# Performance work log

Hardware: AMD Instinct MI355X
Metric: run time of the kernel (lower is better)

Reference implementation:

```python
import jax, jax.numpy as jnp
import numpy as np

N_NODES = 50000
N_EDGES = 800000
IN_CH = 256
H1, D1 = 4, 64   # layer 1: 4 heads x 64 -> 256
H2, D2 = 1, 64   # output layer: 1 head x 64
NEG_SLOPE = 0.2  # DGL GATConv default


def _leaky_relu(x):
    return jnp.where(x >= 0, x, NEG_SLOPE * x)


def gat_conv(h, src, dst, W, attn_l, attn_r, bias, res_W, num_heads, out_feats, apply_elu):
    """DGL GATConv (eval mode, feat_drop=attn_drop=0).
    h: (N, F_in); src/dst: (E,) edge endpoints (edge u->v aggregates at v).
    W: (F_in, H*D); attn_l/attn_r: (H, D); bias: (H*D,); res_W: (F_in, H*D) or None.
    Returns (N, H, D).
    """
    N = h.shape[0]
    ft = (h @ W).reshape(N, num_heads, out_feats)            # (N,H,D)
    el = jnp.sum(ft * attn_l, axis=-1)                        # (N,H)
    er = jnp.sum(ft * attn_r, axis=-1)                        # (N,H)
    e = _leaky_relu(el[src] + er[dst])                        # (E,H)
    # segment softmax over incoming edges of each dst node
    emax = jax.ops.segment_max(e, dst, num_segments=N)        # (N,H)
    emax = jax.lax.stop_gradient(emax)
    ee = jnp.exp(e - emax[dst])                               # (E,H)
    denom = jax.ops.segment_sum(ee, dst, num_segments=N)      # (N,H)
    a = ee / denom[dst]                                       # (E,H)
    msg = ft[src] * a[:, :, None]                             # (E,H,D)
    rst = jax.ops.segment_sum(msg, dst, num_segments=N)       # (N,H,D)
    if res_W is not None:
        rst = rst + (h @ res_W).reshape(N, num_heads, out_feats)
    rst = rst + bias.reshape(num_heads, out_feats)
    if apply_elu:
        rst = jax.nn.elu(rst)
    return rst


def setup_inputs() -> dict:
    key = jax.random.key(0)
    ks = jax.random.split(key, 12)
    feat = jax.random.normal(ks[0], (N_NODES, IN_CH), dtype=jnp.float32)
    src = jax.random.randint(ks[1], (N_EDGES,), 0, N_NODES)
    dst = jax.random.randint(ks[2], (N_EDGES,), 0, N_NODES)
    s = 0.1
    W1 = jax.random.normal(ks[3], (IN_CH, H1 * D1), dtype=jnp.float32) * s
    al1 = jax.random.normal(ks[4], (H1, D1), dtype=jnp.float32) * s
    ar1 = jax.random.normal(ks[5], (H1, D1), dtype=jnp.float32) * s
    b1 = jnp.zeros((H1 * D1,), dtype=jnp.float32)
    W2 = jax.random.normal(ks[6], (H1 * D1, H2 * D2), dtype=jnp.float32) * s
    al2 = jax.random.normal(ks[7], (H2, D2), dtype=jnp.float32) * s
    ar2 = jax.random.normal(ks[8], (H2, D2), dtype=jnp.float32) * s
    b2 = jnp.zeros((H2 * D2,), dtype=jnp.float32)
    resW2 = jax.random.normal(ks[9], (H1 * D1, H2 * D2), dtype=jnp.float32) * s
    return {"feat": feat, "src": src, "dst": dst,
            "W1": W1, "al1": al1, "ar1": ar1, "b1": b1,
            "W2": W2, "al2": al2, "ar2": ar2, "b2": b2, "resW2": resW2}


def reference(feat, src, dst, W1, al1, ar1, b1, W2, al2, ar2, b2, resW2):
    # Layer 1: 4 heads, ELU, no residual (first DGL layer built without residual)
    h = gat_conv(feat, src, dst, W1, al1, ar1, b1, None, H1, D1, True)
    h = h.reshape(N_NODES, H1 * D1)  # flatten(1)
    # Layer 2: 1 head, residual (linear res_fc since 256 != 64), no activation
    h = gat_conv(h, src, dst, W2, al2, ar2, b2, resW2, H2, D2, False)
    return h.mean(axis=1)  # mean over output heads -> (N, out_channels)
```

## Files before the change

### kernel.cpp

```cpp
#include <hip/hip_runtime.h>
#include <math.h>

#define N_NODES 50000
#define N_EDGES 800000
#define ELL_W 64

typedef __attribute__((ext_vector_type(8))) short bf16x8;
typedef __attribute__((ext_vector_type(4))) float f32x4;

__device__ __forceinline__ float leaky(float x) { return x >= 0.f ? x : 0.2f * x; }
__device__ __forceinline__ unsigned short f2bf(float f) {
  unsigned u = __float_as_uint(f);
  return (unsigned short)((u + 0x7fffu + ((u >> 16) & 1u)) >> 16);
}
__device__ __forceinline__ float bflo(unsigned u) { return __uint_as_float(u << 16); }
__device__ __forceinline__ float bfhi(unsigned u) { return __uint_as_float(u & 0xffff0000u); }
__device__ __forceinline__ unsigned pack2(float a, float b) {
  return (unsigned)f2bf(a) | ((unsigned)f2bf(b) << 16);
}

__launch_bounds__(256)
__global__ void prep_k(const float* __restrict__ feat, const float* __restrict__ W1,
                       const float* __restrict__ W2, const float* __restrict__ resW2,
                       short* __restrict__ featb, short* __restrict__ Wt1,
                       short* __restrict__ Wt2) {
  const int gtid = blockIdx.x * 256 + threadIdx.x;
  const int gsz = gridDim.x * 256;
  for (int idx = gtid; idx < 256 * 256; idx += gsz) {
    int n = idx >> 8, k = idx & 255;
    Wt1[idx] = (short)f2bf(W1[(size_t)k * 256 + n]);
  }
  for (int idx = gtid; idx < 128 * 256; idx += gsz) {
    int n = idx >> 8, k = idx & 255;
    float v = (n < 64) ? W2[(size_t)k * 64 + n] : resW2[(size_t)k * 64 + (n - 64)];
    Wt2[idx] = (short)f2bf(v);
  }
  const float4* f4 = (const float4*)feat;
  uint2* fb2 = (uint2*)featb;
  for (int idx = gtid; idx < N_NODES * 64; idx += gsz) {
    float4 f = f4[idx];
    uint2 o;
    o.x = pack2(f.x, f.y);
    o.y = pack2(f.z, f.w);
    fb2[idx] = o;
  }
}

template <int MODE, bool SCAT>
__launch_bounds__(256)
__global__ void mfma_gemm_k(const short* __restrict__ A, const short* __restrict__ Bt,
                            const float* __restrict__ bias, const float* __restrict__ al,
                            const float* __restrict__ ar, float* __restrict__ elp,
                            float* __restrict__ erp, short* __restrict__ Cb,
                            float* __restrict__ Cf, const int* __restrict__ src,
                            const int* __restrict__ dst, int* __restrict__ cnt,
                            int* __restrict__ ell, int M, int K, int N) {
  constexpr int EPI_COLS = (MODE == 0) ? 136 : 72;
  union SharedU {
    struct { short As[4][128][8]; short Bs[4][128][8]; } ab;
    short epi[128 * EPI_COLS];
  };
  __shared__ SharedU sh;

  if (SCAT && blockIdx.y == 2) {
    const int gtid = blockIdx.x * 256 + threadIdx.x;
    const int gsz = gridDim.x * 256;
    for (int e = gtid; e < N_EDGES; e += gsz) {
      int d = dst[e];
      int slot = atomicAdd(cnt + d, 1);
      if (slot < ELL_W) ell[d * ELL_W + slot] = src[e];
    }
    return;
  }
  const int tid = threadIdx.x;
  const int bm0 = blockIdx.x * 128, bn0 = blockIdx.y * 128;
  const int wave = tid >> 6, lane = tid & 63;
  const int wm = (wave & 1) * 64, wn = (wave >> 1) * 64;
  const int q = lane >> 4, r16 = lane & 15;
  const int srow = tid >> 1, sk = (tid & 1) * 16, sq = (tid & 1) * 2;
  f32x4 acc[4][4] = {};

  for (int k0 = 0; k0 < K; k0 += 32) {
    {
      uint4 v0 = {0, 0, 0, 0}, v1 = {0, 0, 0, 0};
      if (bm0 + srow < M) {
        const uint4* p = (const uint4*)(A + (size_t)(bm0 + srow) * K + k0 + sk);
        v0 = p[0];
        v1 = p[1];
      }
      *(uint4*)&sh.ab.As[sq][srow][0] = v0;
      *(uint4*)&sh.ab.As[sq + 1][srow][0] = v1;
    }
    {
      const uint4* p = (const uint4*)(Bt + (size_t)(bn0 + srow) * K + k0 + sk);
      *(uint4*)&sh.ab.Bs[sq][srow][0] = p[0];
      *(uint4*)&sh.ab.Bs[sq + 1][srow][0] = p[1];
    }
    __syncthreads();
    bf16x8 af[4], bfr[4];
#pragma unroll
    for (int i = 0; i < 4; ++i) af[i] = *(const bf16x8*)&sh.ab.As[q][wm + i * 16 + r16][0];
#pragma unroll
    for (int j = 0; j < 4; ++j) bfr[j] = *(const bf16x8*)&sh.ab.Bs[q][wn + j * 16 + r16][0];
#pragma unroll
    for (int i = 0; i < 4; ++i)
#pragma unroll
      for (int j = 0; j < 4; ++j)
        acc[i][j] = __builtin_amdgcn_mfma_f32_16x16x32_bf16(af[i], bfr[j], acc[i][j], 0, 0, 0);
    __syncthreads();
  }

  if (MODE == 0 || wn == 0) {
    const int head = (bn0 + wn) >> 6;
    float alv[4], arv[4];
#pragma unroll
    for (int j = 0; j < 4; ++j) {
      alv[j] = al[((MODE == 0) ? head * 64 : 0) + j * 16 + r16];
      arv[j] = ar[((MODE == 0) ? head * 64 : 0) + j * 16 + r16];
    }
#pragma unroll
    for (int i = 0; i < 4; ++i) {
#pragma unroll
      for (int reg = 0; reg < 4; ++reg) {
        float dl = acc[i][0][reg] * alv[0] + acc[i][1][reg] * alv[1] +
                   acc[i][2][reg] * alv[2] + acc[i][3][reg] * alv[3];
        float dr = acc[i][0][reg] * arv[0] + acc[i][1][reg] * arv[1] +
                   acc[i][2][reg] * arv[2] + acc[i][3][reg] * arv[3];
#pragma unroll
        for (int mm = 1; mm < 16; mm <<= 1) {
          dl += __shfl_xor(dl, mm);
          dr += __shfl_xor(dr, mm);
        }
        int row_g = bm0 + wm + i * 16 + q * 4 + reg;
        if (r16 == 0 && row_g < M) {
          if (MODE == 0) {
            elp[(size_t)row_g * 4 + head] = dl;
            erp[(size_t)row_g * 4 + head] = dr;
          } else {
            elp[row_g] = dl;
            erp[row_g] = dr;
          }
        }
      }
    }
  }

  if (MODE == 0) {
#pragma unroll
    for (int i = 0; i < 4; ++i)
#pragma unroll
      for (int reg = 0; reg < 4; ++reg) {
        int row = wm + i * 16 + q * 4 + reg;
#pragma unroll
        for (int j = 0; j < 4; ++j)
          sh.epi[row * EPI_COLS + wn + j * 16 + r16] = (short)f2bf(acc[i][j][reg]);
      }
    __syncthreads();
#pragma unroll
    for (int k = 0; k < 8; ++k) {
      int c = k * 256 + tid;
      int row = c >> 4, cc = c & 15;
      int row_g = bm0 + row;
      if (row_g < M) {
        uint4 v = *(const uint4*)&sh.epi[row * EPI_COLS + cc * 8];
        *(uint4*)(Cb + (size_t)row_g * N + bn0 + cc * 8) = v;
      }
    }
  } else {
    if (wn == 0) {
#pragma unroll
      for (int i = 0; i < 4; ++i)
#pragma unroll
        for (int reg = 0; reg < 4; ++reg) {
          int row = wm + i * 16 + q * 4 + reg;
#pragma unroll
          for (int j = 0; j < 4; ++j)
            sh.epi[row * EPI_COLS + j * 16 + r16] = (short)f2bf(acc[i][j][reg]);
        }
    } else {
#pragma unroll
      for (int i = 0; i < 4; ++i)
#pragma unroll
        for (int reg = 0; reg < 4; ++reg) {
          int row_g = bm0 + wm + i * 16 + q * 4 + reg;
          if (row_g >= M) continue;
#pragma unroll
          for (int j = 0; j < 4; ++j) {
            int col = j * 16 + r16;
            Cf[(size_t)row_g * 64 + col] = acc[i][j][reg] + bias[col];
          }
        }
    }
    __syncthreads();
#pragma unroll
    for (int k = 0; k < 4; ++k) {
      int c = k * 256 + tid;
      int row = c >> 3, cc = c & 7;
      int row_g = bm0 + row;
      if (row_g < M) {
        uint4 v = *(const uint4*)&sh.epi[row * EPI_COLS + cc * 8];
        *(uint4*)(Cb + (size_t)row_g * 64 + cc * 8) = v;
      }
    }
  }
}

__launch_bounds__(256)
__global__ void agg1_k(const int* __restrict__ ell, const int* __restrict__ cnt,
                       const float* __restrict__ el, const float* __restrict__ er,
                       const short* __restrict__ ft, const float* __restrict__ bias,
                       short* __restrict__ h1) {
  int node = blockIdx.x * 4 + (threadIdx.x >> 6);
  int lane = threadIdx.x & 63;
  if (node >= N_NODES) return;
  int deg = min(cnt[node], ELL_W);
  const int* row = ell + node * ELL_W;
  int h = lane >> 4;
  float erh = er[(size_t)node * 4 + h];
  float denom = 0.f;
  float4 acc = make_float4(0.f, 0.f, 0.f, 0.f);
  int i = 0;
  for (; i + 8 <= deg; i += 8) {
    int s[8];
#pragma unroll
    for (int k = 0; k < 8; ++k) s[k] = row[i + k];
    float e[8];
    uint2 u[8];
#pragma unroll
    for (int k = 0; k < 8; ++k) e[k] = leaky(el[(size_t)s[k] * 4 + h] + erh);
#pragma unroll
    for (int k = 0; k < 8; ++k) u[k] = *(const uint2*)(ft + (size_t)s[k] * 256 + lane * 4);
    float w[8];
#pragma unroll
    for (int k = 0; k < 8; ++k) w[k] = __expf(e[k]);
#pragma unroll
    for (int k = 0; k < 8; ++k) {
      denom += w[k];
      acc.x += w[k] * bflo(u[k].x);
      acc.y += w[k] * bfhi(u[k].x);
      acc.z += w[k] * bflo(u[k].y);
      acc.w += w[k] * bfhi(u[k].y);
    }
  }
  for (; i + 4 <= deg; i += 4) {
    int s0 = row[i + 0], s1 = row[i + 1], s2 = row[i + 2], s3 = row[i + 3];
    float e0 = leaky(el[(size_t)s0 * 4 + h] + erh);
    float e1 = leaky(el[(size_t)s1 * 4 + h] + erh);
    float e2 = leaky(el[(size_t)s2 * 4 + h] + erh);
    float e3 = leaky(el[(size_t)s3 * 4 + h] + erh);
    uint2 u0 = *(const uint2*)(ft + (size_t)s0 * 256 + lane * 4);
    uint2 u1 = *(const uint2*)(ft + (size_t)s1 * 256 + lane * 4);
    uint2 u2 = *(const uint2*)(ft + (size_t)s2 * 256 + lane * 4);
    uint2 u3 = *(const uint2*)(ft + (size_t)s3 * 256 + lane * 4);
    float w0 = __expf(e0), w1 = __expf(e1), w2 = __expf(e2), w3 = __expf(e3);
    denom += (w0 + w1) + (w2 + w3);
    acc.x += (w0 * bflo(u0.x) + w1 * bflo(u1.x)) + (w2 * bflo(u2.x) + w3 * bflo(u3.x));
    acc.y += (w0 * bfhi(u0.x) + w1 * bfhi(u1.x)) + (w2 * bfhi(u2.x) + w3 * bfhi(u3.x));
    acc.z += (w0 * bflo(u0.y) + w1 * bflo(u1.y)) + (w2 * bflo(u2.y) + w3 * bflo(u3.y));
    acc.w += (w0 * bfhi(u0.y) + w1 * bfhi(u1.y)) + (w2 * bfhi(u2.y) + w3 * bfhi(u3.y));
  }
  for (; i < deg; ++i) {
    int s = row[i];
    float e = leaky(el[(size_t)s * 4 + h] + erh);
    uint2 u = *(const uint2*)(ft + (size_t)s * 256 + lane * 4);
    float w = __expf(e);
    denom += w;
    acc.x += w * bflo(u.x);
    acc.y += w * bfhi(u.x);
    acc.z += w * bflo(u.y);
    acc.w += w * bfhi(u.y);
  }
  float inv = (deg > 0) ? 1.f / denom : 0.f;
  float4 b = *(const float4*)(bias + lane * 4);
  float4 v;
  v.x = acc.x * inv + b.x;
  v.y = acc.y * inv + b.y;
  v.z = acc.z * inv + b.z;
  v.w = acc.w * inv + b.w;
  v.x = v.x > 0.f ? v.x : expm1f(v.x);
  v.y = v.y > 0.f ? v.y : expm1f(v.y);
  v.z = v.z > 0.f ? v.z : expm1f(v.z);
  v.w = v.w > 0.f ? v.w : expm1f(v.w);
  uint2 o;
  o.x = pack2(v.x, v.y);
  o.y = pack2(v.z, v.w);
  *(uint2*)(h1 + (size_t)node * 256 + lane * 4) = o;
}

__launch_bounds__(256)
__global__ void agg2_k(const int* __restrict__ ell, const int* __restrict__ cnt,
                       const float* __restrict__ el, const float* __restrict__ er,
                       const short* __restrict__ ft, float* __restrict__ out) {
  int node = blockIdx.x * 4 + (threadIdx.x >> 6);
  int lane = threadIdx.x & 63;
  if (node >= N_NODES) return;
  int deg = min(cnt[node], ELL_W);
  const int* row = ell + node * ELL_W;
  float erd = er[node];
  float denom = 0.f, acc = 0.f;
  int i = 0;
  for (; i + 8 <= deg; i += 8) {
    int s[8];
#pragma unroll
    for (int k = 0; k < 8; ++k) s[k] = row[i + k];
    float e[8], f[8];
#pragma unroll
    for (int k = 0; k < 8; ++k) e[k] = leaky(el[s[k]] + erd);
#pragma unroll
    for (int k = 0; k < 8; ++k)
      f[k] = bflo((unsigned)(unsigned short)ft[(size_t)s[k] * 64 + lane]);
#pragma unroll
    for (int k = 0; k < 8; ++k) {
      float w = __expf(e[k]);
      denom += w;
      acc += w * f[k];
    }
  }
  for (; i < deg; ++i) {
    int s = row[i];
    float e = leaky(el[s] + erd);
    float f = bflo((unsigned)(unsigned short)ft[(size_t)s * 64 + lane]);
    float w = __expf(e);
    denom += w;
    acc += w * f;
  }
  float r = (deg > 0) ? acc / denom : 0.f;
  out[(size_t)node * 64 + lane] += r;
}

extern "C" void kernel_launch(void* const* d_in, const int* in_sizes, int n_in,
                              void* d_out, int out_size, void* d_ws, size_t ws_size,
                              hipStream_t stream) {
  const float* feat  = (const float*)d_in[0];
  const int*   src   = (const int*)d_in[1];
  const int*   dst   = (const int*)d_in[2];
  const float* W1    = (const float*)d_in[3];
  const float* al1   = (const float*)d_in[4];
  const float* ar1   = (const float*)d_in[5];
  const float* b1    = (const float*)d_in[6];
  const float* W2    = (const float*)d_in[7];
  const float* al2   = (const float*)d_in[8];
  const float* ar2   = (const float*)d_in[9];
  const float* b2    = (const float*)d_in[10];
  const float* resW2 = (const float*)d_in[11];
  float* out = (float*)d_out;

  char* p = (char*)d_ws;
  short* featb = (short*)p; p += (size_t)N_NODES * 256 * 2;
  short* ft1b = (short*)p; p += (size_t)N_NODES * 256 * 2;
  short* h1b  = (short*)p; p += (size_t)N_NODES * 256 * 2;
  short* ft2b = (short*)p; p += (size_t)N_NODES * 64 * 2;
  short* Wt1  = (short*)p; p += 256 * 256 * 2;
  short* Wt2  = (short*)p; p += 128 * 256 * 2;
  float* el1  = (float*)p; p += (size_t)N_NODES * 4 * 4;
  float* er1  = (float*)p; p += (size_t)N_NODES * 4 * 4;
  float* el2  = (float*)p; p += (size_t)N_NODES * 4;
  float* er2  = (float*)p; p += (size_t)N_NODES * 4;
  int* cnt    = (int*)p;   p += (size_t)N_NODES * 4;
  int* ell    = (int*)p;   p += (size_t)N_NODES * ELL_W * 4;

  hipMemsetAsync(cnt, 0, (size_t)N_NODES * sizeof(int), stream);

  dim3 blk(256);

  prep_k<<<2048, blk, 0, stream>>>(feat, W1, W2, resW2, featb, Wt1, Wt2);

  mfma_gemm_k<0, true><<<dim3(391, 3), blk, 0, stream>>>(
      featb, Wt1, nullptr, al1, ar1, el1, er1, ft1b, nullptr,
      src, dst, cnt, ell, N_NODES, 256, 256);
  agg1_k<<<12500, blk, 0, stream>>>(ell, cnt, el1, er1, ft1b, b1, h1b);

  mfma_gemm_k<1, false><<<dim3(391, 1), blk, 0, stream>>>(
      h1b, Wt2, b2, al2, ar2, el2, er2, ft2b, out,
      nullptr, nullptr, nullptr, nullptr, N_NODES, 256, 128);
  agg2_k<<<12500, blk, 0, stream>>>(ell, cnt, el2, er2, ft2b, out);
}
```

Before: 288.9 us.

## Split edge scatter across prep and GEMM kernels, store ELL as u16

The edge-to-ELL scatter is split in half: the first half runs in extra blocks of the prep kernel and the second half in the GEMM kernel's spare grid row. The ELL adjacency is stored as 16-bit source indices, which halves its footprint and the index reads in both aggregation kernels. The scatter now handles four edges per thread with vector loads and nontemporal stores. This relies on node ids fitting in 16 bits, and ordering within each ELL row now depends on interleaving across two kernels, which still gives correct results.

```diff
diff --git a/kernel.cpp b/kernel.cpp
--- a/kernel.cpp
+++ b/kernel.cpp
@@ -4,6 +4,10 @@
 #define N_NODES 50000
 #define N_EDGES 800000
 #define ELL_W 64
+
+#define E_SPLIT 400000
+#define CONV_BLKS 1792
+#define SCAT_BLKS 512
 
 typedef __attribute__((ext_vector_type(8))) short bf16x8;
 typedef __attribute__((ext_vector_type(4))) float f32x4;
@@ -19,13 +23,37 @@
   return (unsigned)f2bf(a) | ((unsigned)f2bf(b) << 16);
 }
 
+__device__ __forceinline__ void scat4(const int* __restrict__ src, const int* __restrict__ dst,
+                                      int* __restrict__ cnt, unsigned short* __restrict__ ell,
+                                      int e) {
+  int4 d4 = *(const int4*)(dst + e);
+  int4 s4 = *(const int4*)(src + e);
+  int sl;
+  sl = atomicAdd(cnt + d4.x, 1);
+  if (sl < ELL_W) __builtin_nontemporal_store((unsigned short)s4.x, ell + d4.x * ELL_W + sl);
+  sl = atomicAdd(cnt + d4.y, 1);
+  if (sl < ELL_W) __builtin_nontemporal_store((unsigned short)s4.y, ell + d4.y * ELL_W + sl);
+  sl = atomicAdd(cnt + d4.z, 1);
+  if (sl < ELL_W) __builtin_nontemporal_store((unsigned short)s4.z, ell + d4.z * ELL_W + sl);
+  sl = atomicAdd(cnt + d4.w, 1);
+  if (sl < ELL_W) __builtin_nontemporal_store((unsigned short)s4.w, ell + d4.w * ELL_W + sl);
+}
+
 __launch_bounds__(256)
 __global__ void prep_k(const float* __restrict__ feat, const float* __restrict__ W1,
                        const float* __restrict__ W2, const float* __restrict__ resW2,
                        short* __restrict__ featb, short* __restrict__ Wt1,
-                       short* __restrict__ Wt2) {
+                       short* __restrict__ Wt2, const int* __restrict__ src,
+                       const int* __restrict__ dst, int* __restrict__ cnt,
+                       unsigned short* __restrict__ ell) {
+  if (blockIdx.x >= CONV_BLKS) {
+    const int gtid = (blockIdx.x - CONV_BLKS) * 256 + threadIdx.x;
+    const int gsz = SCAT_BLKS * 256;
+    for (int q = gtid; q < E_SPLIT / 4; q += gsz) scat4(src, dst, cnt, ell, q * 4);
+    return;
+  }
   const int gtid = blockIdx.x * 256 + threadIdx.x;
-  const int gsz = gridDim.x * 256;
+  const int gsz = CONV_BLKS * 256;
   for (int idx = gtid; idx < 256 * 256; idx += gsz) {
     int n = idx >> 8, k = idx & 255;
     Wt1[idx] = (short)f2bf(W1[(size_t)k * 256 + n]);
@@ -54,7 +82,7 @@
                             float* __restrict__ erp, short* __restrict__ Cb,
                             float* __restrict__ Cf, const int* __restrict__ src,
                             const int* __restrict__ dst, int* __restrict__ cnt,
-                            int* __restrict__ ell, int M, int K, int N) {
+                            unsigned short* __restrict__ ell, int M, int K, int N) {
   constexpr int EPI_COLS = (MODE == 0) ? 136 : 72;
   union SharedU {
     struct { short As[4][128][8]; short Bs[4][128][8]; } ab;
@@ -65,11 +93,8 @@
   if (SCAT && blockIdx.y == 2) {
     const int gtid = blockIdx.x * 256 + threadIdx.x;
     const int gsz = gridDim.x * 256;
-    for (int e = gtid; e < N_EDGES; e += gsz) {
-      int d = dst[e];
-      int slot = atomicAdd(cnt + d, 1);
-      if (slot < ELL_W) ell[d * ELL_W + slot] = src[e];
-    }
+    for (int q = gtid; q < (N_EDGES - E_SPLIT) / 4; q += gsz)
+      scat4(src, dst, cnt, ell, E_SPLIT + q * 4);
     return;
   }
   const int tid = threadIdx.x;
@@ -206,7 +231,7 @@
 }
 
 __launch_bounds__(256)
-__global__ void agg1_k(const int* __restrict__ ell, const int* __restrict__ cnt,
+__global__ void agg1_k(const unsigned short* __restrict__ ell, const int* __restrict__ cnt,
                        const float* __restrict__ el, const float* __restrict__ er,
                        const short* __restrict__ ft, const float* __restrict__ bias,
                        short* __restrict__ h1) {
@@ -214,7 +239,7 @@
   int lane = threadIdx.x & 63;
   if (node >= N_NODES) return;
   int deg = min(cnt[node], ELL_W);
-  const int* row = ell + node * ELL_W;
+  const unsigned short* row = ell + node * ELL_W;
   int h = lane >> 4;
   float erh = er[(size_t)node * 4 + h];
   float denom = 0.f;
@@ -288,14 +313,14 @@
 }
 
 __launch_bounds__(256)
-__global__ void agg2_k(const int* __restrict__ ell, const int* __restrict__ cnt,
+__global__ void agg2_k(const unsigned short* __restrict__ ell, const int* __restrict__ cnt,
                        const float* __restrict__ el, const float* __restrict__ er,
                        const short* __restrict__ ft, float* __restrict__ out) {
   int node = blockIdx.x * 4 + (threadIdx.x >> 6);
   int lane = threadIdx.x & 63;
   if (node >= N_NODES) return;
   int deg = min(cnt[node], ELL_W);
-  const int* row = ell + node * ELL_W;
+  const unsigned short* row = ell + node * ELL_W;
   float erd = er[node];
   float denom = 0.f, acc = 0.f;
   int i = 0;
@@ -357,13 +382,14 @@
   float* el2  = (float*)p; p += (size_t)N_NODES * 4;
   float* er2  = (float*)p; p += (size_t)N_NODES * 4;
   int* cnt    = (int*)p;   p += (size_t)N_NODES * 4;
-  int* ell    = (int*)p;   p += (size_t)N_NODES * ELL_W * 4;
+  unsigned short* ell = (unsigned short*)p; p += (size_t)N_NODES * ELL_W * 2;
 
   hipMemsetAsync(cnt, 0, (size_t)N_NODES * sizeof(int), stream);
 
   dim3 blk(256);
 
-  prep_k<<<2048, blk, 0, stream>>>(feat, W1, W2, resW2, featb, Wt1, Wt2);
+  prep_k<<<CONV_BLKS + SCAT_BLKS, blk, 0, stream>>>(feat, W1, W2, resW2, featb, Wt1, Wt2,
+                                                    src, dst, cnt, ell);
 
   mfma_gemm_k<0, true><<<dim3(391, 3), blk, 0, stream>>>(
       featb, Wt1, nullptr, al1, ar1, el1, er1, ft1b, nullptr,
```

Measured after the change: 289.7 us. No clear change (+0.3%).
